# Performance work log

Hardware: AMD Instinct MI355X
Metric: run time of the kernel (lower is better)

The kernel has to match this reference:

```python
import jax, jax.numpy as jnp
import numpy as np

GAMMA = 0.1
ENERGY = 0.5
BATCH = 64
INF = 1e10  # finite 'infinity' so exp(-INF/gamma) underflows to exactly 0


def softdtw_batch(D, gamma):
    """Batched soft-DTW over pairwise frame-distance matrices.
    D: [P, T, T] squared-Euclidean distances. Returns R(T-1,T-1): [P].
    DP is parallelized across anti-diagonals (wavefront)."""
    P, T, _ = D.shape
    iarr = jnp.arange(T)

    def body(carry, k):
        Rm2, Rm1 = carry  # diagonals k-2 and k-1, each [P, T] indexed by row i
        j = k - iarr
        valid = (j >= 0) & (j < T)
        d = D[:, iarr, jnp.clip(j, 0, T - 1)]  # [P, T]
        pad = jnp.full((P, 1), INF, D.dtype)
        r_up = jnp.concatenate([pad, Rm1[:, :-1]], axis=1)      # R(i-1, j)
        r_left = Rm1                                            # R(i, j-1)
        corner = jnp.where(k == 0, jnp.float32(0.0), jnp.float32(INF))
        r_diag = jnp.concatenate([jnp.full((P, 1), 1.0, D.dtype) * corner,
                                  Rm2[:, :-1]], axis=1)         # R(i-1, j-1)
        z = jnp.stack([r_up, r_left, r_diag], axis=0)           # [3, P, T]
        smin = -gamma * jax.nn.logsumexp(-z / gamma, axis=0)
        Rk = jnp.where(valid[None, :], d + smin, INF)
        return (Rm1, Rk), None

    init = (jnp.full((P, T), INF, D.dtype), jnp.full((P, T), INF, D.dtype))
    (_, Rlast), _ = jax.lax.scan(body, init, jnp.arange(2 * T - 1))
    return Rlast[:, T - 1]


def setup_inputs() -> dict:
    key = jax.random.key(0)
    k1, k2 = jax.random.split(key)
    xxx = jax.random.normal(k1, (BATCH, 64, 13), dtype=jnp.float32)
    yyy = jax.random.normal(k2, (BATCH, 64, 13), dtype=jnp.float32)
    return {"xxx": xxx, "yyy": yyy}


def reference(xxx, yyy):
    B = BATCH
    full = jnp.concatenate([xxx, yyy], axis=0)  # [N, T, d]
    N, T, _ = full.shape
    # pairwise squared-Euclidean frame distances: [N, N, T, T]
    sq = jnp.sum(full * full, axis=-1)                      # [N, T]
    dots = jnp.einsum('aid,bjd->abij', full, full)          # [N, N, T, T]
    D = sq[:, None, :, None] + sq[None, :, None, :] - 2.0 * dots
    R = softdtw_batch(D.reshape(N * N, T, T), GAMMA)        # [N*N]
    sim = R.reshape(N, N)
    eye = jnp.eye(N, dtype=bool)
    sim = jnp.where(eye, 0.0, sim)  # i==j pairs skipped in original (left as 0)
    sim = sim / ENERGY
    pos = jnp.diagonal(sim, offset=B)                       # [B]
    positives = jnp.concatenate([pos, pos], axis=0)         # [2B] (source uses +B offset twice)
    loss = jnp.mean(-positives + jax.nn.logsumexp(sim, axis=-1))
    return loss
```

## Files before the change

kernel.cpp:

```cpp
#include <hip/hip_runtime.h>

#define TT 64
#define DIM 13
#define NSEQ 128
#define NPAIRS 8128
#define INFV 1e10f
#define C_EXP 14.4269504088896f
#define C_INV 0.06931471805599453f

typedef _Float16 h2 __attribute__((ext_vector_type(2)));

__device__ __forceinline__ float fdot2(h2 a, h2 b, float c) {
#if __has_builtin(__builtin_amdgcn_fdot2)
    return __builtin_amdgcn_fdot2(a, b, c, false);
#else
    return c + (float)a.x * (float)b.x + (float)a.y * (float)b.y;
#endif
}
__device__ __forceinline__ h2 mkh2(float a, float b) {
    h2 p; p.x = (_Float16)a; p.y = (_Float16)b; return p;
}

__global__ __launch_bounds__(256) void sdtw_pairs(const float* __restrict__ xxx,
                                                  const float* __restrict__ yyy,
                                                  float* __restrict__ simR) {
    __shared__ unsigned xl[7 * 4 * TT];
    const int wave = threadIdx.x >> 6;
    const int lane = threadIdx.x & 63;
    const int t = blockIdx.x * 4 + wave;

    int a = (int)((255.0f - sqrtf(65025.0f - 8.0f * (float)t)) * 0.5f);
    if (a < 0) a = 0;
    if (a > 126) a = 126;
    while (a * (255 - a) / 2 > t) a--;
    while ((a + 1) * (254 - a) / 2 <= t) a++;
    const int b = a + 1 + (t - a * (255 - a) / 2);

    const float* fb = ((b < 64) ? xxx + (size_t)b * TT * DIM
                                : yyy + (size_t)(b - 64) * TT * DIM) + lane * DIM;
    float sqy = 0.f, yv[DIM];
#pragma unroll
    for (int c = 0; c < DIM; c++) { yv[c] = fb[c]; sqy += yv[c] * yv[c]; }
    h2 yh[7];
#pragma unroll
    for (int c = 0; c < 6; c++) yh[c] = mkh2(yv[2 * c], yv[2 * c + 1]);
    yh[6] = mkh2(yv[12], 1.0f);

    {
        const float* fx = ((a < 64) ? xxx + (size_t)a * TT * DIM
                                    : yyy + (size_t)(a - 64) * TT * DIM) + lane * DIM;
        float xv[DIM], sqx = 0.f;
#pragma unroll
        for (int c = 0; c < DIM; c++) { xv[c] = fx[c]; sqx += xv[c] * xv[c]; }
        unsigned* row = xl + wave * TT + lane;
#pragma unroll
        for (int c = 0; c < 6; c++)
            row[c * 256] = __builtin_bit_cast(unsigned, mkh2(-2.f * xv[2 * c], -2.f * xv[2 * c + 1]));
        row[6 * 256] = __builtin_bit_cast(unsigned, mkh2(-2.f * xv[12], sqx));
    }
    __syncthreads();

    const unsigned* xw = xl + wave * TT;
    float S = INFV;
    float dgc = (lane == 0) ? 0.f : INFV;
    const bool lane0 = (lane == 0);
    int jc = (-lane) & (TT - 1);

#pragma unroll 4
    for (int k = 0; k < 2 * TT - 1; k++) {
        float acc = sqy;
        acc = fdot2(yh[0], __builtin_bit_cast(h2, xw[jc]),            acc);
        acc = fdot2(yh[1], __builtin_bit_cast(h2, xw[jc + 1 * 256]),  acc);
        acc = fdot2(yh[2], __builtin_bit_cast(h2, xw[jc + 2 * 256]),  acc);
        acc = fdot2(yh[3], __builtin_bit_cast(h2, xw[jc + 3 * 256]),  acc);
        acc = fdot2(yh[4], __builtin_bit_cast(h2, xw[jc + 4 * 256]),  acc);
        acc = fdot2(yh[5], __builtin_bit_cast(h2, xw[jc + 5 * 256]),  acc);
        acc = fdot2(yh[6], __builtin_bit_cast(h2, xw[jc + 6 * 256]),  acc);
        jc = (jc + 1) & (TT - 1);

        float lf = __shfl_up(S, 1);
        lf = lane0 ? INFV : lf;
        float up = S;

        float m   = fminf(fminf(up, lf), dgc);
        float med = __builtin_amdgcn_fmed3f(up, lf, dgc);
        float M   = fmaxf(fmaxf(up, lf), dgc);
        float sum = 1.0f + __builtin_amdgcn_exp2f(m - med)
                         + __builtin_amdgcn_exp2f(m - M);
        S = fmaf(acc, C_EXP, m - __builtin_amdgcn_logf(sum));
        dgc = lf;
    }

    if (lane == 63) {
        const float r = S * C_INV;
        simR[a * NSEQ + b] = r;
        simR[b * NSEQ + a] = r;
    }
}

__global__ void row_lse(float* __restrict__ simR) {
    const int r = blockIdx.x;
    const int lane = threadIdx.x;
    const float* rowp = simR + r * NSEQ;
    float v0 = (lane == r) ? 0.f : 2.f * rowp[lane];
    const int c1 = lane + 64;
    float v1 = (c1 == r) ? 0.f : 2.f * rowp[c1];
    float mx = fmaxf(v0, v1);
#pragma unroll
    for (int o = 32; o; o >>= 1) mx = fmaxf(mx, __shfl_xor(mx, o));
    float s = __builtin_amdgcn_exp2f((v0 - mx) * 1.4426950408889634f)
            + __builtin_amdgcn_exp2f((v1 - mx) * 1.4426950408889634f);
#pragma unroll
    for (int o = 32; o; o >>= 1) s += __shfl_xor(s, o);
    if (lane == 0) {
        const int i = r & 63;
        float pos = 2.f * simR[i * NSEQ + i + 64];
        simR[r * NSEQ + r] = mx + 0.6931471805599453f * __builtin_amdgcn_logf(s) - pos;
    }
}

__global__ void final_loss(const float* __restrict__ simR, float* __restrict__ out) {
    __shared__ float red[NSEQ];
    const int tid = threadIdx.x;
    red[tid] = simR[tid * NSEQ + tid];
    __syncthreads();
    if (tid == 0) {
        float tsum = 0.f;
        for (int c = 0; c < NSEQ; c++) tsum += red[c];
        out[0] = tsum * (1.0f / NSEQ);
    }
}

extern "C" void kernel_launch(void* const* d_in, const int* in_sizes, int n_in,
                              void* d_out, int out_size, void* d_ws, size_t ws_size,
                              hipStream_t stream) {
    const float* xxx = (const float*)d_in[0];
    const float* yyy = (const float*)d_in[1];
    float* out = (float*)d_out;
    float* simR = (float*)d_ws;

    sdtw_pairs<<<NPAIRS / 4, 256, 0, stream>>>(xxx, yyy, simR);
    row_lse<<<NSEQ, 64, 0, stream>>>(simR);
    final_loss<<<1, NSEQ, 0, stream>>>(simR, out);
}
```

Measured before the change: 51.98 us.

## Process two pairs per wave sharing x row, use DPP row shift

Each wave now computes two soft-DTW recurrences that share the same sequence a, so the LDS loads of the x features are reused across both pairs and the two independent dependency chains interleave to hide latency. The grid halves to 4096 waves with a new pair-indexing scheme. The lane shift-up uses a DPP row_shr with INF fill instead of shfl_up plus select. The DPP row_shr:1 only shifts within 16-lane rows, so lanes 16, 32 and 48 get INF instead of their neighbour, which risks wrong results. It also duplicates the work for a=126 where b2==b1.

```diff
diff --git a/kernel.cpp b/kernel.cpp
--- a/kernel.cpp
+++ b/kernel.cpp
@@ -3,7 +3,7 @@
 #define TT 64
 #define DIM 13
 #define NSEQ 128
-#define NPAIRS 8128
+#define NWAVE 4096
 #define INFV 1e10f
 #define C_EXP 14.4269504088896f
 #define C_INV 0.06931471805599453f
@@ -20,6 +20,12 @@
 __device__ __forceinline__ h2 mkh2(float a, float b) {
     h2 p; p.x = (_Float16)a; p.y = (_Float16)b; return p;
 }
+__device__ __forceinline__ float shr1_inf(float x) {
+    int r = __builtin_amdgcn_update_dpp(__builtin_bit_cast(int, INFV),
+                                        __builtin_bit_cast(int, x),
+                                        0x138, 0xf, 0xf, false);
+    return __builtin_bit_cast(float, r);
+}
 
 __global__ __launch_bounds__(256) void sdtw_pairs(const float* __restrict__ xxx,
                                                   const float* __restrict__ yyy,
@@ -29,22 +35,36 @@
     const int lane = threadIdx.x & 63;
     const int t = blockIdx.x * 4 + wave;
 
-    int a = (int)((255.0f - sqrtf(65025.0f - 8.0f * (float)t)) * 0.5f);
+    int a = 128 - (int)sqrtf(16384.0f - 4.0f * (float)t);
     if (a < 0) a = 0;
     if (a > 126) a = 126;
-    while (a * (255 - a) / 2 > t) a--;
-    while ((a + 1) * (254 - a) / 2 <= t) a++;
-    const int b = a + 1 + (t - a * (255 - a) / 2);
+    while (64 * a - ((a * a) >> 2) > t) a--;
+    while (64 * (a + 1) - (((a + 1) * (a + 1)) >> 2) <= t) a++;
+    const int q = t - (64 * a - ((a * a) >> 2));
+    const int b1 = a + 1 + 2 * q;
+    const int b2 = (b1 < 127) ? b1 + 1 : b1;
 
-    const float* fb = ((b < 64) ? xxx + (size_t)b * TT * DIM
-                                : yyy + (size_t)(b - 64) * TT * DIM) + lane * DIM;
-    float sqy = 0.f, yv[DIM];
+    h2 yh1[7], yh2[7];
+    float sqy1 = 0.f, sqy2 = 0.f;
+    {
+        const float* f1 = ((b1 < 64) ? xxx + (size_t)b1 * TT * DIM
+                                     : yyy + (size_t)(b1 - 64) * TT * DIM) + lane * DIM;
+        const float* f2 = ((b2 < 64) ? xxx + (size_t)b2 * TT * DIM
+                                     : yyy + (size_t)(b2 - 64) * TT * DIM) + lane * DIM;
+        float v1[DIM], v2[DIM];
 #pragma unroll
-    for (int c = 0; c < DIM; c++) { yv[c] = fb[c]; sqy += yv[c] * yv[c]; }
-    h2 yh[7];
+        for (int c = 0; c < DIM; c++) {
+            v1[c] = f1[c]; sqy1 += v1[c] * v1[c];
+            v2[c] = f2[c]; sqy2 += v2[c] * v2[c];
+        }
 #pragma unroll
-    for (int c = 0; c < 6; c++) yh[c] = mkh2(yv[2 * c], yv[2 * c + 1]);
-    yh[6] = mkh2(yv[12], 1.0f);
+        for (int c = 0; c < 6; c++) {
+            yh1[c] = mkh2(v1[2 * c], v1[2 * c + 1]);
+            yh2[c] = mkh2(v2[2 * c], v2[2 * c + 1]);
+        }
+        yh1[6] = mkh2(v1[12], 1.0f);
+        yh2[6] = mkh2(v2[12], 1.0f);
+    }
 
     {
         const float* fx = ((a < 64) ? xxx + (size_t)a * TT * DIM
@@ -61,40 +81,62 @@
     __syncthreads();
 
     const unsigned* xw = xl + wave * TT;
-    float S = INFV;
-    float dgc = (lane == 0) ? 0.f : INFV;
-    const bool lane0 = (lane == 0);
+    float S1 = INFV, S2 = INFV;
+    float dg1 = (lane == 0) ? 0.f : INFV;
+    float dg2 = dg1;
     int jc = (-lane) & (TT - 1);
 
-#pragma unroll 4
+#pragma unroll 2
     for (int k = 0; k < 2 * TT - 1; k++) {
-        float acc = sqy;
-        acc = fdot2(yh[0], __builtin_bit_cast(h2, xw[jc]),            acc);
-        acc = fdot2(yh[1], __builtin_bit_cast(h2, xw[jc + 1 * 256]),  acc);
-        acc = fdot2(yh[2], __builtin_bit_cast(h2, xw[jc + 2 * 256]),  acc);
-        acc = fdot2(yh[3], __builtin_bit_cast(h2, xw[jc + 3 * 256]),  acc);
-        acc = fdot2(yh[4], __builtin_bit_cast(h2, xw[jc + 4 * 256]),  acc);
-        acc = fdot2(yh[5], __builtin_bit_cast(h2, xw[jc + 5 * 256]),  acc);
-        acc = fdot2(yh[6], __builtin_bit_cast(h2, xw[jc + 6 * 256]),  acc);
+        unsigned w0 = xw[jc];
+        unsigned w1 = xw[jc + 1 * 256];
+        unsigned w2 = xw[jc + 2 * 256];
+        unsigned w3 = xw[jc + 3 * 256];
+        unsigned w4 = xw[jc + 4 * 256];
+        unsigned w5 = xw[jc + 5 * 256];
+        unsigned w6 = xw[jc + 6 * 256];
         jc = (jc + 1) & (TT - 1);
 
-        float lf = __shfl_up(S, 1);
-        lf = lane0 ? INFV : lf;
-        float up = S;
+        float acc1 = sqy1, acc2 = sqy2;
+        acc1 = fdot2(yh1[0], __builtin_bit_cast(h2, w0), acc1);
+        acc2 = fdot2(yh2[0], __builtin_bit_cast(h2, w0), acc2);
+        acc1 = fdot2(yh1[1], __builtin_bit_cast(h2, w1), acc1);
+        acc2 = fdot2(yh2[1], __builtin_bit_cast(h2, w1), acc2);
+        acc1 = fdot2(yh1[2], __builtin_bit_cast(h2, w2), acc1);
+        acc2 = fdot2(yh2[2], __builtin_bit_cast(h2, w2), acc2);
+        acc1 = fdot2(yh1[3], __builtin_bit_cast(h2, w3), acc1);
+        acc2 = fdot2(yh2[3], __builtin_bit_cast(h2, w3), acc2);
+        acc1 = fdot2(yh1[4], __builtin_bit_cast(h2, w4), acc1);
+        acc2 = fdot2(yh2[4], __builtin_bit_cast(h2, w4), acc2);
+        acc1 = fdot2(yh1[5], __builtin_bit_cast(h2, w5), acc1);
+        acc2 = fdot2(yh2[5], __builtin_bit_cast(h2, w5), acc2);
+        acc1 = fdot2(yh1[6], __builtin_bit_cast(h2, w6), acc1);
+        acc2 = fdot2(yh2[6], __builtin_bit_cast(h2, w6), acc2);
 
-        float m   = fminf(fminf(up, lf), dgc);
-        float med = __builtin_amdgcn_fmed3f(up, lf, dgc);
-        float M   = fmaxf(fmaxf(up, lf), dgc);
-        float sum = 1.0f + __builtin_amdgcn_exp2f(m - med)
-                         + __builtin_amdgcn_exp2f(m - M);
-        S = fmaf(acc, C_EXP, m - __builtin_amdgcn_logf(sum));
-        dgc = lf;
+        float lf1 = shr1_inf(S1);
+        float lf2 = shr1_inf(S2);
+
+        float m1   = fminf(fminf(S1, lf1), dg1);
+        float m2   = fminf(fminf(S2, lf2), dg2);
+        float md1  = __builtin_amdgcn_fmed3f(S1, lf1, dg1);
+        float md2  = __builtin_amdgcn_fmed3f(S2, lf2, dg2);
+        float M1   = fmaxf(fmaxf(S1, lf1), dg1);
+        float M2   = fmaxf(fmaxf(S2, lf2), dg2);
+        float sum1 = 1.0f + __builtin_amdgcn_exp2f(m1 - md1) + __builtin_amdgcn_exp2f(m1 - M1);
+        float sum2 = 1.0f + __builtin_amdgcn_exp2f(m2 - md2) + __builtin_amdgcn_exp2f(m2 - M2);
+        S1 = fmaf(acc1, C_EXP, m1 - __builtin_amdgcn_logf(sum1));
+        S2 = fmaf(acc2, C_EXP, m2 - __builtin_amdgcn_logf(sum2));
+        dg1 = lf1;
+        dg2 = lf2;
     }
 
     if (lane == 63) {
-        const float r = S * C_INV;
-        simR[a * NSEQ + b] = r;
-        simR[b * NSEQ + a] = r;
+        const float r1 = S1 * C_INV;
+        const float r2 = S2 * C_INV;
+        simR[a * NSEQ + b1] = r1;
+        simR[b1 * NSEQ + a] = r1;
+        simR[a * NSEQ + b2] = r2;
+        simR[b2 * NSEQ + a] = r2;
     }
 }
 
@@ -139,7 +181,7 @@
     float* out = (float*)d_out;
     float* simR = (float*)d_ws;
 
-    sdtw_pairs<<<NPAIRS / 4, 256, 0, stream>>>(xxx, yyy, simR);
+    sdtw_pairs<<<NWAVE / 4, 256, 0, stream>>>(xxx, yyy, simR);
     row_lse<<<NSEQ, 64, 0, stream>>>(simR);
     final_loss<<<1, NSEQ, 0, stream>>>(simR, out);
 }
```

Result: faster. 50.27 us (-3.3%).

## Process four soft-DTW pairs per wave sharing one row sequence

Applied to the files above, without the earlier changes.

Each wave now runs four independent soft-DTW recurrences that share the same 'a' sequence. The shared x data is loaded from LDS once per step and reused across four dot products. Interleaving four chains is meant to hide the latency of the serial exp/log dependency and to cut LDS reads per pair. The lane shuffle is replaced with a DPP row shift that fills INF at the boundary, and min/max use v_min3/v_max3. Padding pairs at the end of a row recompute duplicates (clamped to 127). Blocks shrink to one wave, which raises register pressure and reduces the number of waves in flight.

```diff
diff --git a/kernel.cpp b/kernel.cpp
--- a/kernel.cpp
+++ b/kernel.cpp
@@ -3,7 +3,7 @@
 #define TT 64
 #define DIM 13
 #define NSEQ 128
-#define NPAIRS 8128
+#define NWAVE 2080
 #define INFV 1e10f
 #define C_EXP 14.4269504088896f
 #define C_INV 0.06931471805599453f
@@ -11,90 +11,168 @@
 typedef _Float16 h2 __attribute__((ext_vector_type(2)));
 
 __device__ __forceinline__ float fdot2(h2 a, h2 b, float c) {
-#if __has_builtin(__builtin_amdgcn_fdot2)
     return __builtin_amdgcn_fdot2(a, b, c, false);
-#else
-    return c + (float)a.x * (float)b.x + (float)a.y * (float)b.y;
-#endif
 }
 __device__ __forceinline__ h2 mkh2(float a, float b) {
     h2 p; p.x = (_Float16)a; p.y = (_Float16)b; return p;
 }
-
-__global__ __launch_bounds__(256) void sdtw_pairs(const float* __restrict__ xxx,
-                                                  const float* __restrict__ yyy,
-                                                  float* __restrict__ simR) {
-    __shared__ unsigned xl[7 * 4 * TT];
-    const int wave = threadIdx.x >> 6;
-    const int lane = threadIdx.x & 63;
-    const int t = blockIdx.x * 4 + wave;
-
-    int a = (int)((255.0f - sqrtf(65025.0f - 8.0f * (float)t)) * 0.5f);
+__device__ __forceinline__ h2 bch2(unsigned u) { return __builtin_bit_cast(h2, u); }
+__device__ __forceinline__ float shr1_inf(float x) {
+    int r = __builtin_amdgcn_update_dpp(__builtin_bit_cast(int, INFV),
+                                        __builtin_bit_cast(int, x),
+                                        0x138, 0xf, 0xf, false);
+    return __builtin_bit_cast(float, r);
+}
+__device__ __forceinline__ float min3f(float a, float b, float c) {
+    float d; asm("v_min3_f32 %0, %1, %2, %3" : "=v"(d) : "v"(a), "v"(b), "v"(c)); return d;
+}
+__device__ __forceinline__ float max3f(float a, float b, float c) {
+    float d; asm("v_max3_f32 %0, %1, %2, %3" : "=v"(d) : "v"(a), "v"(b), "v"(c)); return d;
+}
+__device__ __forceinline__ int Tq(int N) {
+    int q = N >> 2, r = N & 3;
+    return 2 * q * (q + 1) + r * (q + 1);
+}
+
+__global__ __launch_bounds__(64, 2) void sdtw_pairs(const float* __restrict__ xxx,
+                                                    const float* __restrict__ yyy,
+                                                    float* __restrict__ simR) {
+    __shared__ unsigned xl[7 * TT];
+    const int lane = threadIdx.x;
+    const int t = blockIdx.x;
+
+    int a = 127 - (int)sqrtf(8.0f * (float)(NWAVE - t));
     if (a < 0) a = 0;
     if (a > 126) a = 126;
-    while (a * (255 - a) / 2 > t) a--;
-    while ((a + 1) * (254 - a) / 2 <= t) a++;
-    const int b = a + 1 + (t - a * (255 - a) / 2);
-
-    const float* fb = ((b < 64) ? xxx + (size_t)b * TT * DIM
-                                : yyy + (size_t)(b - 64) * TT * DIM) + lane * DIM;
-    float sqy = 0.f, yv[DIM];
-#pragma unroll
-    for (int c = 0; c < DIM; c++) { yv[c] = fb[c]; sqy += yv[c] * yv[c]; }
-    h2 yh[7];
-#pragma unroll
-    for (int c = 0; c < 6; c++) yh[c] = mkh2(yv[2 * c], yv[2 * c + 1]);
-    yh[6] = mkh2(yv[12], 1.0f);
-
+    while (NWAVE - Tq(127 - a) > t) a--;
+    while (a < 126 && NWAVE - Tq(127 - (a + 1)) <= t) a++;
+    const int q4 = t - (NWAVE - Tq(127 - a));
+    const int b0 = a + 1 + 4 * q4;
+    const int bA = b0;
+    const int bB = (b0 + 1 < 128) ? b0 + 1 : 127;
+    const int bC = (b0 + 2 < 128) ? b0 + 2 : 127;
+    const int bD = (b0 + 3 < 128) ? b0 + 3 : 127;
+
+    h2 yA[7], yB[7], yC[7], yD[7];
+    float sqA = 0.f, sqB = 0.f, sqC = 0.f, sqD = 0.f;
     {
-        const float* fx = ((a < 64) ? xxx + (size_t)a * TT * DIM
-                                    : yyy + (size_t)(a - 64) * TT * DIM) + lane * DIM;
+        const float* fA = ((bA < 64) ? xxx + (size_t)bA * TT * DIM : yyy + (size_t)(bA - 64) * TT * DIM) + lane * DIM;
+        const float* fB = ((bB < 64) ? xxx + (size_t)bB * TT * DIM : yyy + (size_t)(bB - 64) * TT * DIM) + lane * DIM;
+        const float* fC = ((bC < 64) ? xxx + (size_t)bC * TT * DIM : yyy + (size_t)(bC - 64) * TT * DIM) + lane * DIM;
+        const float* fD = ((bD < 64) ? xxx + (size_t)bD * TT * DIM : yyy + (size_t)(bD - 64) * TT * DIM) + lane * DIM;
+        float vA[DIM], vB[DIM], vC[DIM], vD[DIM];
+#pragma unroll
+        for (int c = 0; c < DIM; c++) {
+            vA[c] = fA[c]; sqA += vA[c] * vA[c];
+            vB[c] = fB[c]; sqB += vB[c] * vB[c];
+            vC[c] = fC[c]; sqC += vC[c] * vC[c];
+            vD[c] = fD[c]; sqD += vD[c] * vD[c];
+        }
+#pragma unroll
+        for (int c = 0; c < 6; c++) {
+            yA[c] = mkh2(vA[2 * c], vA[2 * c + 1]);
+            yB[c] = mkh2(vB[2 * c], vB[2 * c + 1]);
+            yC[c] = mkh2(vC[2 * c], vC[2 * c + 1]);
+            yD[c] = mkh2(vD[2 * c], vD[2 * c + 1]);
+        }
+        yA[6] = mkh2(vA[12], 1.0f);
+        yB[6] = mkh2(vB[12], 1.0f);
+        yC[6] = mkh2(vC[12], 1.0f);
+        yD[6] = mkh2(vD[12], 1.0f);
+    }
+
+    {
+        const float* fx = ((a < 64) ? xxx + (size_t)a * TT * DIM : yyy + (size_t)(a - 64) * TT * DIM) + lane * DIM;
         float xv[DIM], sqx = 0.f;
 #pragma unroll
         for (int c = 0; c < DIM; c++) { xv[c] = fx[c]; sqx += xv[c] * xv[c]; }
-        unsigned* row = xl + wave * TT + lane;
 #pragma unroll
         for (int c = 0; c < 6; c++)
-            row[c * 256] = __builtin_bit_cast(unsigned, mkh2(-2.f * xv[2 * c], -2.f * xv[2 * c + 1]));
-        row[6 * 256] = __builtin_bit_cast(unsigned, mkh2(-2.f * xv[12], sqx));
+            xl[c * TT + lane] = __builtin_bit_cast(unsigned, mkh2(-2.f * xv[2 * c], -2.f * xv[2 * c + 1]));
+        xl[6 * TT + lane] = __builtin_bit_cast(unsigned, mkh2(-2.f * xv[12], sqx));
     }
     __syncthreads();
 
-    const unsigned* xw = xl + wave * TT;
-    float S = INFV;
-    float dgc = (lane == 0) ? 0.f : INFV;
-    const bool lane0 = (lane == 0);
+    float SA = INFV, SB = INFV, SC = INFV, SD = INFV;
+    const float ini = (lane == 0) ? 0.f : INFV;
+    float dA = ini, dB = ini, dC = ini, dD = ini;
     int jc = (-lane) & (TT - 1);
 
-#pragma unroll 4
+#pragma unroll 2
     for (int k = 0; k < 2 * TT - 1; k++) {
-        float acc = sqy;
-        acc = fdot2(yh[0], __builtin_bit_cast(h2, xw[jc]),            acc);
-        acc = fdot2(yh[1], __builtin_bit_cast(h2, xw[jc + 1 * 256]),  acc);
-        acc = fdot2(yh[2], __builtin_bit_cast(h2, xw[jc + 2 * 256]),  acc);
-        acc = fdot2(yh[3], __builtin_bit_cast(h2, xw[jc + 3 * 256]),  acc);
-        acc = fdot2(yh[4], __builtin_bit_cast(h2, xw[jc + 4 * 256]),  acc);
-        acc = fdot2(yh[5], __builtin_bit_cast(h2, xw[jc + 5 * 256]),  acc);
-        acc = fdot2(yh[6], __builtin_bit_cast(h2, xw[jc + 6 * 256]),  acc);
+        unsigned w0 = xl[jc];
+        unsigned w1 = xl[jc + 1 * TT];
+        unsigned w2 = xl[jc + 2 * TT];
+        unsigned w3 = xl[jc + 3 * TT];
+        unsigned w4 = xl[jc + 4 * TT];
+        unsigned w5 = xl[jc + 5 * TT];
+        unsigned w6 = xl[jc + 6 * TT];
         jc = (jc + 1) & (TT - 1);
 
-        float lf = __shfl_up(S, 1);
-        lf = lane0 ? INFV : lf;
-        float up = S;
-
-        float m   = fminf(fminf(up, lf), dgc);
-        float med = __builtin_amdgcn_fmed3f(up, lf, dgc);
-        float M   = fmaxf(fmaxf(up, lf), dgc);
-        float sum = 1.0f + __builtin_amdgcn_exp2f(m - med)
-                         + __builtin_amdgcn_exp2f(m - M);
-        S = fmaf(acc, C_EXP, m - __builtin_amdgcn_logf(sum));
-        dgc = lf;
+        float aA = sqA, aB = sqB, aC = sqC, aD = sqD;
+        aA = fdot2(yA[0], bch2(w0), aA); aB = fdot2(yB[0], bch2(w0), aB);
+        aC = fdot2(yC[0], bch2(w0), aC); aD = fdot2(yD[0], bch2(w0), aD);
+        aA = fdot2(yA[1], bch2(w1), aA); aB = fdot2(yB[1], bch2(w1), aB);
+        aC = fdot2(yC[1], bch2(w1), aC); aD = fdot2(yD[1], bch2(w1), aD);
+        aA = fdot2(yA[2], bch2(w2), aA); aB = fdot2(yB[2], bch2(w2), aB);
+        aC = fdot2(yC[2], bch2(w2), aC); aD = fdot2(yD[2], bch2(w2), aD);
+        aA = fdot2(yA[3], bch2(w3), aA); aB = fdot2(yB[3], bch2(w3), aB);
+        aC = fdot2(yC[3], bch2(w3), aC); aD = fdot2(yD[3], bch2(w3), aD);
+        aA = fdot2(yA[4], bch2(w4), aA); aB = fdot2(yB[4], bch2(w4), aB);
+        aC = fdot2(yC[4], bch2(w4), aC); aD = fdot2(yD[4], bch2(w4), aD);
+        aA = fdot2(yA[5], bch2(w5), aA); aB = fdot2(yB[5], bch2(w5), aB);
+        aC = fdot2(yC[5], bch2(w5), aC); aD = fdot2(yD[5], bch2(w5), aD);
+        aA = fdot2(yA[6], bch2(w6), aA); aB = fdot2(yB[6], bch2(w6), aB);
+        aC = fdot2(yC[6], bch2(w6), aC); aD = fdot2(yD[6], bch2(w6), aD);
+
+        float lA = shr1_inf(SA);
+        float lB = shr1_inf(SB);
+        float lC = shr1_inf(SC);
+        float lD = shr1_inf(SD);
+
+        {
+            float m = min3f(SA, lA, dA);
+            float md = __builtin_amdgcn_fmed3f(SA, lA, dA);
+            float M = max3f(SA, lA, dA);
+            float s = 1.0f + __builtin_amdgcn_exp2f(m - md) + __builtin_amdgcn_exp2f(m - M);
+            SA = fmaf(aA, C_EXP, m - __builtin_amdgcn_logf(s));
+            dA = lA;
+        }
+        {
+            float m = min3f(SB, lB, dB);
+            float md = __builtin_amdgcn_fmed3f(SB, lB, dB);
+            float M = max3f(SB, lB, dB);
+            float s = 1.0f + __builtin_amdgcn_exp2f(m - md) + __builtin_amdgcn_exp2f(m - M);
+            SB = fmaf(aB, C_EXP, m - __builtin_amdgcn_logf(s));
+            dB = lB;
+        }
+        {
+            float m = min3f(SC, lC, dC);
+            float md = __builtin_amdgcn_fmed3f(SC, lC, dC);
+            float M = max3f(SC, lC, dC);
+            float s = 1.0f + __builtin_amdgcn_exp2f(m - md) + __builtin_amdgcn_exp2f(m - M);
+            SC = fmaf(aC, C_EXP, m - __builtin_amdgcn_logf(s));
+            dC = lC;
+        }
+        {
+            float m = min3f(SD, lD, dD);
+            float md = __builtin_amdgcn_fmed3f(SD, lD, dD);
+            float M = max3f(SD, lD, dD);
+            float s = 1.0f + __builtin_amdgcn_exp2f(m - md) + __builtin_amdgcn_exp2f(m - M);
+            SD = fmaf(aD, C_EXP, m - __builtin_amdgcn_logf(s));
+            dD = lD;
+        }
     }
 
     if (lane == 63) {
-        const float r = S * C_INV;
-        simR[a * NSEQ + b] = r;
-        simR[b * NSEQ + a] = r;
+        const float rA = SA * C_INV;
+        const float rB = SB * C_INV;
+        const float rC = SC * C_INV;
+        const float rD = SD * C_INV;
+        simR[a * NSEQ + bA] = rA; simR[bA * NSEQ + a] = rA;
+        simR[a * NSEQ + bB] = rB; simR[bB * NSEQ + a] = rB;
+        simR[a * NSEQ + bC] = rC; simR[bC * NSEQ + a] = rC;
+        simR[a * NSEQ + bD] = rD; simR[bD * NSEQ + a] = rD;
     }
 }
 
@@ -139,7 +217,7 @@
     float* out = (float*)d_out;
     float* simR = (float*)d_ws;
 
-    sdtw_pairs<<<NPAIRS / 4, 256, 0, stream>>>(xxx, yyy, simR);
+    sdtw_pairs<<<NWAVE, 64, 0, stream>>>(xxx, yyy, simR);
     row_lse<<<NSEQ, 64, 0, stream>>>(simR);
     final_loss<<<1, NSEQ, 0, stream>>>(simR, out);
 }
```

Result: slower. 75.16 us (+44.6%).

## Pack two soft-DTW pairs per wave with two columns per lane

Applied to the files above, without the earlier changes.

Each wave now processes two sequence pairs, one per 32-lane half, and each lane owns two adjacent columns of the DP. The wavefront takes 95 steps instead of 127, and each x-frame LDS load feeds two dot products. The cross-lane shift now uses a DPP row_shr with an INF fill in place of the shuffle. Each step's two soft-min updates depend on each other, so the serial chain per step gets longer, and half the waves are launched.

```diff
diff --git a/kernel.cpp b/kernel.cpp
--- a/kernel.cpp
+++ b/kernel.cpp
@@ -4,6 +4,8 @@
 #define DIM 13
 #define NSEQ 128
 #define NPAIRS 8128
+#define NWAVE 4064
+#define NSTEP (TT + 32 - 1)
 #define INFV 1e10f
 #define C_EXP 14.4269504088896f
 #define C_INV 0.06931471805599453f
@@ -11,88 +13,120 @@
 typedef _Float16 h2 __attribute__((ext_vector_type(2)));
 
 __device__ __forceinline__ float fdot2(h2 a, h2 b, float c) {
-#if __has_builtin(__builtin_amdgcn_fdot2)
     return __builtin_amdgcn_fdot2(a, b, c, false);
-#else
-    return c + (float)a.x * (float)b.x + (float)a.y * (float)b.y;
-#endif
 }
 __device__ __forceinline__ h2 mkh2(float a, float b) {
     h2 p; p.x = (_Float16)a; p.y = (_Float16)b; return p;
+}
+__device__ __forceinline__ h2 bch2(unsigned u) { return __builtin_bit_cast(h2, u); }
+__device__ __forceinline__ float shr1_inf(float x) {
+    int r = __builtin_amdgcn_update_dpp(__builtin_bit_cast(int, INFV),
+                                        __builtin_bit_cast(int, x),
+                                        0x138, 0xf, 0xf, false);
+    return __builtin_bit_cast(float, r);
+}
+__device__ __forceinline__ float smstep(float S, float lf, float dg, float acc) {
+    float m  = fminf(fminf(S, lf), dg);
+    float md = __builtin_amdgcn_fmed3f(S, lf, dg);
+    float M  = fmaxf(fmaxf(S, lf), dg);
+    float s  = 1.0f + __builtin_amdgcn_exp2f(m - md) + __builtin_amdgcn_exp2f(m - M);
+    return fmaf(acc, C_EXP, m - __builtin_amdgcn_logf(s));
 }
 
 __global__ __launch_bounds__(256) void sdtw_pairs(const float* __restrict__ xxx,
                                                   const float* __restrict__ yyy,
                                                   float* __restrict__ simR) {
-    __shared__ unsigned xl[7 * 4 * TT];
+    __shared__ unsigned xl[4][7 * 2 * TT];
     const int wave = threadIdx.x >> 6;
     const int lane = threadIdx.x & 63;
-    const int t = blockIdx.x * 4 + wave;
+    const int half = lane >> 5;
+    const int sj   = lane & 31;
+    const int p = 2 * (blockIdx.x * 4 + wave) + half;
 
-    int a = (int)((255.0f - sqrtf(65025.0f - 8.0f * (float)t)) * 0.5f);
+    int a = (int)((255.0f - sqrtf(65025.0f - 8.0f * (float)p)) * 0.5f);
     if (a < 0) a = 0;
     if (a > 126) a = 126;
-    while (a * (255 - a) / 2 > t) a--;
-    while ((a + 1) * (254 - a) / 2 <= t) a++;
-    const int b = a + 1 + (t - a * (255 - a) / 2);
+    while (a * (255 - a) / 2 > p) a--;
+    while ((a + 1) * (254 - a) / 2 <= p) a++;
+    const int b = a + 1 + (p - a * (255 - a) / 2);
 
-    const float* fb = ((b < 64) ? xxx + (size_t)b * TT * DIM
-                                : yyy + (size_t)(b - 64) * TT * DIM) + lane * DIM;
-    float sqy = 0.f, yv[DIM];
+    h2 yA[7], yB[7];
+    float sqyA = 0.f, sqyB = 0.f;
+    {
+        const float* fb = ((b < 64) ? xxx + (size_t)b * TT * DIM
+                                    : yyy + (size_t)(b - 64) * TT * DIM) + (2 * sj) * DIM;
+        float vA[DIM], vB[DIM];
 #pragma unroll
-    for (int c = 0; c < DIM; c++) { yv[c] = fb[c]; sqy += yv[c] * yv[c]; }
-    h2 yh[7];
+        for (int c = 0; c < DIM; c++) {
+            vA[c] = fb[c];        sqyA += vA[c] * vA[c];
+            vB[c] = fb[DIM + c];  sqyB += vB[c] * vB[c];
+        }
 #pragma unroll
-    for (int c = 0; c < 6; c++) yh[c] = mkh2(yv[2 * c], yv[2 * c + 1]);
-    yh[6] = mkh2(yv[12], 1.0f);
+        for (int c = 0; c < 6; c++) {
+            yA[c] = mkh2(vA[2 * c], vA[2 * c + 1]);
+            yB[c] = mkh2(vB[2 * c], vB[2 * c + 1]);
+        }
+        yA[6] = mkh2(vA[12], 1.0f);
+        yB[6] = mkh2(vB[12], 1.0f);
+    }
 
     {
-        const float* fx = ((a < 64) ? xxx + (size_t)a * TT * DIM
-                                    : yyy + (size_t)(a - 64) * TT * DIM) + lane * DIM;
-        float xv[DIM], sqx = 0.f;
+        const float* fa = (a < 64) ? xxx + (size_t)a * TT * DIM
+                                   : yyy + (size_t)(a - 64) * TT * DIM;
+        unsigned* xw = xl[wave];
 #pragma unroll
-        for (int c = 0; c < DIM; c++) { xv[c] = fx[c]; sqx += xv[c] * xv[c]; }
-        unsigned* row = xl + wave * TT + lane;
+        for (int rr = 0; rr < 2; rr++) {
+            const int r = sj + 32 * rr;
+            const float* fx = fa + r * DIM;
+            float xv[DIM], sqx = 0.f;
 #pragma unroll
-        for (int c = 0; c < 6; c++)
-            row[c * 256] = __builtin_bit_cast(unsigned, mkh2(-2.f * xv[2 * c], -2.f * xv[2 * c + 1]));
-        row[6 * 256] = __builtin_bit_cast(unsigned, mkh2(-2.f * xv[12], sqx));
+            for (int c = 0; c < DIM; c++) { xv[c] = fx[c]; sqx += xv[c] * xv[c]; }
+            unsigned* dst = xw + half * TT + r;
+#pragma unroll
+            for (int c = 0; c < 6; c++)
+                dst[c * 128] = __builtin_bit_cast(unsigned, mkh2(-2.f * xv[2 * c], -2.f * xv[2 * c + 1]));
+            dst[6 * 128] = __builtin_bit_cast(unsigned, mkh2(-2.f * xv[12], sqx));
+        }
     }
     __syncthreads();
 
-    const unsigned* xw = xl + wave * TT;
-    float S = INFV;
-    float dgc = (lane == 0) ? 0.f : INFV;
-    const bool lane0 = (lane == 0);
-    int jc = (-lane) & (TT - 1);
+    const unsigned* xp = xl[wave] + half * TT;
+    float SA = INFV, SB = INFV;
+    float dgA = (sj == 0) ? 0.f : INFV;
+    const bool col0 = (sj == 0);
+    int ic = (-sj) & (TT - 1);
 
-#pragma unroll 4
-    for (int k = 0; k < 2 * TT - 1; k++) {
-        float acc = sqy;
-        acc = fdot2(yh[0], __builtin_bit_cast(h2, xw[jc]),            acc);
-        acc = fdot2(yh[1], __builtin_bit_cast(h2, xw[jc + 1 * 256]),  acc);
-        acc = fdot2(yh[2], __builtin_bit_cast(h2, xw[jc + 2 * 256]),  acc);
-        acc = fdot2(yh[3], __builtin_bit_cast(h2, xw[jc + 3 * 256]),  acc);
-        acc = fdot2(yh[4], __builtin_bit_cast(h2, xw[jc + 4 * 256]),  acc);
-        acc = fdot2(yh[5], __builtin_bit_cast(h2, xw[jc + 5 * 256]),  acc);
-        acc = fdot2(yh[6], __builtin_bit_cast(h2, xw[jc + 6 * 256]),  acc);
-        jc = (jc + 1) & (TT - 1);
+#pragma unroll 2
+    for (int k = 0; k < NSTEP; k++) {
+        unsigned w0 = xp[ic];
+        unsigned w1 = xp[ic + 1 * 128];
+        unsigned w2 = xp[ic + 2 * 128];
+        unsigned w3 = xp[ic + 3 * 128];
+        unsigned w4 = xp[ic + 4 * 128];
+        unsigned w5 = xp[ic + 5 * 128];
+        unsigned w6 = xp[ic + 6 * 128];
+        ic = (ic + 1) & (TT - 1);
 
-        float lf = __shfl_up(S, 1);
-        lf = lane0 ? INFV : lf;
-        float up = S;
+        float aA = sqyA, aB = sqyB;
+        aA = fdot2(yA[0], bch2(w0), aA); aB = fdot2(yB[0], bch2(w0), aB);
+        aA = fdot2(yA[1], bch2(w1), aA); aB = fdot2(yB[1], bch2(w1), aB);
+        aA = fdot2(yA[2], bch2(w2), aA); aB = fdot2(yB[2], bch2(w2), aB);
+        aA = fdot2(yA[3], bch2(w3), aA); aB = fdot2(yB[3], bch2(w3), aB);
+        aA = fdot2(yA[4], bch2(w4), aA); aB = fdot2(yB[4], bch2(w4), aB);
+        aA = fdot2(yA[5], bch2(w5), aA); aB = fdot2(yB[5], bch2(w5), aB);
+        aA = fdot2(yA[6], bch2(w6), aA); aB = fdot2(yB[6], bch2(w6), aB);
 
-        float m   = fminf(fminf(up, lf), dgc);
-        float med = __builtin_amdgcn_fmed3f(up, lf, dgc);
-        float M   = fmaxf(fmaxf(up, lf), dgc);
-        float sum = 1.0f + __builtin_amdgcn_exp2f(m - med)
-                         + __builtin_amdgcn_exp2f(m - M);
-        S = fmaf(acc, C_EXP, m - __builtin_amdgcn_logf(sum));
-        dgc = lf;
+        float lfA = shr1_inf(SB);
+        lfA = col0 ? INFV : lfA;
+
+        float SAold = SA;
+        SA = smstep(SA, lfA, dgA, aA);
+        SB = smstep(SB, SA, SAold, aB);
+        dgA = lfA;
     }
 
-    if (lane == 63) {
-        const float r = S * C_INV;
+    if (sj == 31) {
+        const float r = SB * C_INV;
         simR[a * NSEQ + b] = r;
         simR[b * NSEQ + a] = r;
     }
@@ -127,7 +161,7 @@
     if (tid == 0) {
         float tsum = 0.f;
         for (int c = 0; c < NSEQ; c++) tsum += red[c];
-        out[0] = tsum * (1.0f / NSEQ);
+        out[0] = tsum / (float)NSEQ;
     }
 }
 
@@ -139,7 +173,7 @@
     float* out = (float*)d_out;
     float* simR = (float*)d_ws;
 
-    sdtw_pairs<<<NPAIRS / 4, 256, 0, stream>>>(xxx, yyy, simR);
+    sdtw_pairs<<<NWAVE / 4, 256, 0, stream>>>(xxx, yyy, simR);
     row_lse<<<NSEQ, 64, 0, stream>>>(simR);
     final_loss<<<1, NSEQ, 0, stream>>>(simR, out);
 }
```

New measurement: 42.13 us, median of 2. -18.9%, faster.
